# Performance work log

Measured on AMD Instinct MI355X. Metric: run time of the kernel, lower is better.

The kernel has to match this reference:

```python
import jax, jax.numpy as jnp
import numpy as np

D = 128      # entity_and_theorem_embedding_size
M = 8192     # nodes per tree level
L = 5        # internal (non-leaf) levels
V = 4096     # number of input entities (leaf vocab)
K = 8        # number of binary numerical functions
KL = 4       # number of binary logic functions
G = 4096     # number of ground-truth logic statements


def setup_inputs() -> dict:
    key = jax.random.key(0)
    ks = jax.random.split(key, 16)
    s = 0.05
    return {
        "leaf_ids": jax.random.randint(ks[0], (M,), 0, V, dtype=jnp.int32),
        "left_idx": jax.random.randint(ks[1], (L, M), 0, M, dtype=jnp.int32),
        "right_idx": jax.random.randint(ks[2], (L, M), 0, M, dtype=jnp.int32),
        "nf_fid": jax.random.randint(ks[3], (L, M), 0, K, dtype=jnp.int32),
        "gt_left": jax.random.randint(ks[4], (G,), 0, M, dtype=jnp.int32),
        "gt_right": jax.random.randint(ks[5], (G,), 0, M, dtype=jnp.int32),
        "lf_fid": jax.random.randint(ks[6], (G,), 0, KL, dtype=jnp.int32),
        "emb": jax.random.normal(ks[7], (V, D), jnp.float32),
        "W1": jax.random.normal(ks[8], (K, 2 * D, 4 * D), jnp.float32) * s,
        "b1": jnp.zeros((K, 4 * D), jnp.float32),
        "W2": jax.random.normal(ks[9], (K, 4 * D, 2 * D), jnp.float32) * s,
        "b2": jnp.zeros((K, 2 * D), jnp.float32),
        "W3": jax.random.normal(ks[10], (K, 2 * D, D), jnp.float32) * s,
        "b3": jnp.zeros((K, D), jnp.float32),
        "Wl1": jax.random.normal(ks[11], (KL, 2 * D, 4 * D), jnp.float32) * s,
        "bl1": jnp.zeros((KL, 4 * D), jnp.float32),
        "Wl2": jax.random.normal(ks[12], (KL, 4 * D, D), jnp.float32) * s,
        "bl2": jnp.zeros((KL, D), jnp.float32),
    }


def _select(y, fid):
    # y: [N, K, F], fid: [N] -> [N, F]  (per-node dynamic MLP dispatch)
    return jnp.take_along_axis(y, fid[:, None, None], axis=1)[:, 0, :]


def reference(leaf_ids, left_idx, right_idx, nf_fid, gt_left, gt_right, lf_fid,
              emb, W1, b1, W2, b2, W3, b3, Wl1, bl1, Wl2, bl2):
    # Leaf entities: embedding lookup (input_entity_embedding)
    h0 = emb[leaf_ids]  # [M, D]

    # Internal entity nodes: recursive nf_two2one MLPs, level-synchronous
    def level(h, xs):
        li, ri, fid = xs
        x = jnp.concatenate([h[li], h[ri]], axis=-1)          # [M, 2D] concat of operands
        a1 = jax.nn.relu(jnp.einsum('nd,kdf->nkf', x, W1) + b1)   # [M, K, 4D]
        a2 = jax.nn.relu(jnp.einsum('nkd,kdf->nkf', a1, W2) + b2) # [M, K, 2D]
        a3 = jnp.einsum('nkd,kdf->nkf', a2, W3) + b3              # [M, K, D]
        return _select(a3, fid), None
    hL, _ = jax.lax.scan(level, h0, (left_idx, right_idx, nf_fid))

    # Logic statements: lf_two2one MLP on pairs of entity encodings
    xg = jnp.concatenate([hL[gt_left], hL[gt_right]], axis=-1)    # [G, 2D]
    g1 = jax.nn.relu(jnp.einsum('nd,kdf->nkf', xg, Wl1) + bl1)    # [G, KL, 4D]
    g2 = jnp.einsum('nkd,kdf->nkf', g1, Wl2) + bl2                # [G, KL, D]
    return _select(g2, lf_fid)                                    # [G, D]
```

## Files before the change

### kernel.cpp

```cpp
#include <hip/hip_runtime.h>

constexpr int D  = 128;
constexpr int M  = 8192;
constexpr int L  = 5;
constexpr int K  = 8;
constexpr int KL = 4;
constexpr int G  = 4096;

constexpr int TB   = 64;
constexpr int PADL = M + K * TB;
constexpr int PADG = G + KL * TB;

typedef short bf16x8 __attribute__((ext_vector_type(8)));
typedef float f32x4  __attribute__((ext_vector_type(4)));

__device__ __forceinline__ unsigned short f2bf(float x) {
  union { float f; unsigned int u; } c; c.f = x;
  unsigned int u = c.u + 0x7FFF + ((c.u >> 16) & 1);
  return (unsigned short)(u >> 16);
}
__device__ __forceinline__ float bf2f(unsigned short h) {
  union { unsigned int u; float f; } c; c.u = ((unsigned int)h) << 16;
  return c.f;
}

__global__ void leaf_gather_kernel(const int* __restrict__ leaf_ids,
                                   const float* __restrict__ emb,
                                   short* __restrict__ hs) {
  int idx = blockIdx.x * 256 + threadIdx.x;
  int n = idx >> 7, d = idx & 127;
  float w = emb[(size_t)leaf_ids[n] * D + d];
  unsigned short hh = f2bf(w);
  hs[n * 256 + d]       = (short)hh;
  hs[n * 256 + 128 + d] = (short)f2bf(w - bf2f(hh));
}

__global__ void bucket64_kernel(const int* __restrict__ nf_fid,
                                const int* __restrict__ lf_fid,
                                int* __restrict__ orders) {
  int b = blockIdx.x;
  const int* fid; int N, Kf, cap; int* out;
  if (b < L) { fid = nf_fid + b * M; N = M; Kf = K;  cap = PADL; out = orders + b * PADL; }
  else       { fid = lf_fid;         N = G; Kf = KL; cap = PADG; out = orders + L * PADL; }
  __shared__ int cnt[8];
  __shared__ int cur[8];
  int tid = threadIdx.x;
  if (tid < Kf) cnt[tid] = 0;
  __syncthreads();
  for (int i = tid; i < N; i += 256) atomicAdd(&cnt[fid[i]], 1);
  __syncthreads();
  if (tid == 0) {
    int off = 0;
    for (int k = 0; k < Kf; ++k) { cur[k] = off; off += ((cnt[k] + TB - 1) / TB) * TB; }
  }
  __syncthreads();
  for (int i = tid; i < cap; i += 256) out[i] = -1;
  __syncthreads();
  for (int i = tid; i < N; i += 256) {
    int kk = fid[i];
    int pos = atomicAdd(&cur[kk], 1);
    out[pos] = i;
  }
}

__global__ void prep_kernel(const float* __restrict__ W1, const float* __restrict__ W2,
                            const float* __restrict__ W3, const float* __restrict__ Wl1,
                            const float* __restrict__ Wl2,
                            short* __restrict__ B1T, short* __restrict__ B2T,
                            short* __restrict__ B3T, short* __restrict__ BL1T,
                            short* __restrict__ BL2T) {
  int b = blockIdx.x;
  const float* W; short* BT; int KD, F;
  if      (b < 4096) { W = W1;  BT = B1T;  KD = 256; F = 512; }
  else if (b < 6144) { W = W2;  BT = B2T;  KD = 512; F = 256; b -= 4096; }
  else if (b < 7168) { W = W3;  BT = B3T;  KD = 256; F = 128; b -= 6144; }
  else if (b < 9216) { W = Wl1; BT = BL1T; KD = 256; F = 512; b -= 7168; }
  else               { W = Wl2; BT = BL2T; KD = 512; F = 128; b -= 9216; }
  int k = b / F, f = b % F;
  for (int d = threadIdx.x; d < KD; d += 256) {
    float w = W[((size_t)k * KD + d) * F + f];
    unsigned short hi = f2bf(w);
    unsigned short lo = f2bf(w - bf2f(hi));
    BT[((size_t)k * F + f) * (2 * KD) + d]      = (short)hi;
    BT[((size_t)k * F + f) * (2 * KD) + KD + d] = (short)lo;
  }
}

template<int KH, int NN, int EPI, int FUSED>
__global__ __launch_bounds__(256, 3) void mfma_gemm(
    const short* __restrict__ A, const short* __restrict__ hsrc,
    const int* __restrict__ gl, const int* __restrict__ gr,
    const short* __restrict__ BT, const float* __restrict__ bias,
    short* __restrict__ Aout, float* __restrict__ outp,
    const int* __restrict__ order, const int* __restrict__ fid) {
  constexpr int BK    = 64;
  constexpr int NCH   = 3 * KH / BK;
  constexpr int LDA   = BK + 8;
  constexpr int TROWS = 32;
  __shared__ __align__(16) short As[2][TROWS * LDA];
  __shared__ __align__(16) short Bs[2][128 * LDA];
  __shared__ int nodesS[TROWS], liS[TROWS], riS[TROWS];

  const int tid  = threadIdx.x;
  const int row0 = blockIdx.x * TROWS;
  const int ct   = blockIdx.y;

  if (tid < TROWS) {
    int node = order[row0 + tid];
    nodesS[tid] = node;
    if (FUSED) {
      liS[tid] = node >= 0 ? gl[node] : 0;
      riS[tid] = node >= 0 ? gr[node] : 0;
    }
  }
  __syncthreads();
  if (nodesS[0] < 0) return;
  const int kfn = fid[nodesS[0]];
  const short* __restrict__ Bk = BT + (size_t)kfn * NN * (2 * KH);

  const int lane = tid & 63, wave = tid >> 6;
  const int wr = (wave >> 1) * 16;
  const int wc = wave & 1;
  const int l15 = lane & 15, oct = lane >> 4;

  const int ar = tid >> 3;
  const int ag = (tid & 7) * 8;
  const int bn = tid >> 1;
  const int bg = (tid & 1) * 32;

  f32x4 acc[4];
  #pragma unroll
  for (int j = 0; j < 4; ++j) acc[j] = (f32x4)0.f;

  auto loadB_to = [&](int c, int4& r0, int4& r1, int4& r2, int4& r3) {
    int ko = c * BK, seg = ko / KH, wi = ko % KH;
    int pb = (seg == 2) ? KH + wi : wi;
    const int4* p = (const int4*)(Bk + (size_t)(ct * 128 + bn) * (2 * KH) + pb + bg);
    r0 = p[0]; r1 = p[1]; r2 = p[2]; r3 = p[3];
  };
  auto loadA_to = [&](int c, int4& r0) {
    int ko = c * BK, seg = ko / KH, wi = ko % KH;
    int pa = ((seg == 1) ? KH : 0) + wi + ag;
    if (FUSED) {
      int s4 = pa >> 7;
      int node = (s4 & 1) ? riS[ar] : liS[ar];
      if (nodesS[ar] >= 0) {
        r0 = *(const int4*)(hsrc + (size_t)node * 256 + ((s4 >> 1) << 7) + (pa & 127));
      } else {
        r0 = make_int4(0, 0, 0, 0);
      }
    } else {
      r0 = *(const int4*)(A + (size_t)(row0 + ar) * (2 * KH) + pa);
    }
  };
  auto storeA = [&](int b, const int4& r0) {
    *(int4*)&As[b][ar * LDA + ag] = r0;
  };
  auto storeB = [&](int b, const int4& r0, const int4& r1, const int4& r2, const int4& r3) {
    int4* db = (int4*)&Bs[b][bn * LDA + bg];
    db[0] = r0; db[1] = r1; db[2] = r2; db[3] = r3;
  };
  auto compute = [&](int b) {
    __builtin_amdgcn_s_setprio(1);
    #pragma unroll
    for (int s = 0; s < 2; ++s) {
      const int ko = s * 32 + oct * 8;
      bf16x8 afr = *(const bf16x8*)&As[b][(wr + l15) * LDA + ko];
      #pragma unroll
      for (int cf = 0; cf < 4; ++cf) {
        bf16x8 bb = *(const bf16x8*)&Bs[b][(wc * 64 + cf * 16 + l15) * LDA + ko];
        acc[cf] = __builtin_amdgcn_mfma_f32_16x16x32_bf16(afr, bb, acc[cf], 0, 0, 0);
      }
    }
    __builtin_amdgcn_s_setprio(0);
  };

  int4 a0, a1, b00, b01, b02, b03, b10, b11, b12, b13;
  loadA_to(0, a0); loadB_to(0, b00, b01, b02, b03);
  loadA_to(1, a1); loadB_to(1, b10, b11, b12, b13);
  storeA(0, a0); storeB(0, b00, b01, b02, b03);
  __syncthreads();
  for (int c = 0; c < NCH; c += 2) {
    storeA(1, a1); storeB(1, b10, b11, b12, b13);
    if (c + 2 < NCH) { loadA_to(c + 2, a0); loadB_to(c + 2, b00, b01, b02, b03); }
    compute(0);
    __syncthreads();
    if (c + 2 < NCH) { storeA(0, a0); storeB(0, b00, b01, b02, b03); }
    if (c + 3 < NCH) { loadA_to(c + 3, a1); loadB_to(c + 3, b10, b11, b12, b13); }
    compute(1);
    __syncthreads();
  }

  if (EPI == 0) {
    short* Ls = (short*)&Bs[0][0];
    #pragma unroll
    for (int part = 0; part < 2; ++part) {
      __syncthreads();
      #pragma unroll
      for (int cf = 0; cf < 4; ++cf) {
        int colL = wc * 64 + cf * 16 + l15;
        float bv = bias[kfn * NN + ct * 128 + colL];
        #pragma unroll
        for (int j = 0; j < 4; ++j) {
          int row = wr + oct * 4 + j;
          float v = fmaxf(acc[cf][j] + bv, 0.f);
          unsigned short hh = f2bf(v);
          unsigned short val = (part == 0) ? hh : f2bf(v - bf2f(hh));
          Ls[row * 128 + colL] = (short)val;
        }
      }
      __syncthreads();
      int row = tid >> 3, sg = (tid & 7) * 16;
      const int4* src = (const int4*)&Ls[row * 128 + sg];
      int4* dst = (int4*)&Aout[(size_t)(row0 + row) * (2 * NN) + part * NN + ct * 128 + sg];
      dst[0] = src[0]; dst[1] = src[1];
    }
  } else if (EPI == 1) {
    float* Lf = (float*)&Bs[0][0];
    #pragma unroll
    for (int h = 0; h < 2; ++h) {
      __syncthreads();
      if (wc == h) {
        #pragma unroll
        for (int cf = 0; cf < 4; ++cf) {
          int colL = cf * 16 + l15;
          float bv = bias[kfn * 128 + h * 64 + colL];
          #pragma unroll
          for (int j = 0; j < 4; ++j) {
            int row = wr + oct * 4 + j;
            Lf[row * 64 + colL] = acc[cf][j] + bv;
          }
        }
      }
      __syncthreads();
      int row = tid >> 3, off = (tid & 7) * 8;
      int node = nodesS[row];
      if (node >= 0) {
        const float4* src = (const float4*)&Lf[row * 64 + off];
        float4* dst = (float4*)&outp[(size_t)node * 128 + h * 64 + off];
        dst[0] = src[0]; dst[1] = src[1];
      }
    }
  } else {
    short* Ls = (short*)&Bs[0][0];
    #pragma unroll
    for (int cf = 0; cf < 4; ++cf) {
      int colL = wc * 64 + cf * 16 + l15;
      float bv = bias[kfn * 128 + colL];
      #pragma unroll
      for (int j = 0; j < 4; ++j) {
        int row = wr + oct * 4 + j;
        float v = acc[cf][j] + bv;
        unsigned short hh = f2bf(v);
        Ls[row * 256 + colL]       = (short)hh;
        Ls[row * 256 + 128 + colL] = (short)f2bf(v - bf2f(hh));
      }
    }
    __syncthreads();
    int row = tid >> 3, sg = (tid & 7) * 32;
    int node = nodesS[row];
    if (node >= 0) {
      const int4* src = (const int4*)&Ls[row * 256 + sg];
      int4* dst = (int4*)&Aout[(size_t)node * 256 + sg];
      dst[0] = src[0]; dst[1] = src[1]; dst[2] = src[2]; dst[3] = src[3];
    }
  }
}

extern "C" void kernel_launch(void* const* d_in, const int* in_sizes, int n_in,
                              void* d_out, int out_size, void* d_ws, size_t ws_size,
                              hipStream_t stream) {
  const int*   leaf_ids  = (const int*)d_in[0];
  const int*   left_idx  = (const int*)d_in[1];
  const int*   right_idx = (const int*)d_in[2];
  const int*   nf_fid    = (const int*)d_in[3];
  const int*   gt_left   = (const int*)d_in[4];
  const int*   gt_right  = (const int*)d_in[5];
  const int*   lf_fid    = (const int*)d_in[6];
  const float* emb       = (const float*)d_in[7];
  const float* W1 = (const float*)d_in[8];
  const float* b1 = (const float*)d_in[9];
  const float* W2 = (const float*)d_in[10];
  const float* b2 = (const float*)d_in[11];
  const float* W3 = (const float*)d_in[12];
  const float* b3 = (const float*)d_in[13];
  const float* Wl1 = (const float*)d_in[14];
  const float* bl1 = (const float*)d_in[15];
  const float* Wl2 = (const float*)d_in[16];
  const float* bl2 = (const float*)d_in[17];
  float* out = (float*)d_out;

  const size_t SZ_H    = (size_t)M * 256 * 2;
  const size_t SZ_A1   = (size_t)PADL * 1024 * 2;
  const size_t SZ_A2   = (size_t)PADL * 512 * 2;
  const size_t SZ_B1T  = (size_t)8 * 512 * 512 * 2;
  const size_t SZ_B2T  = (size_t)8 * 256 * 1024 * 2;
  const size_t SZ_B3T  = (size_t)8 * 128 * 512 * 2;
  const size_t SZ_BL1T = (size_t)4 * 512 * 512 * 2;
  const size_t SZ_BL2T = (size_t)4 * 128 * 1024 * 2;

  char* p = (char*)d_ws;
  short* hsA  = (short*)p;  p += SZ_H;
  short* hsB  = (short*)p;  p += SZ_H;
  short* a1s  = (short*)p;  p += SZ_A1;
  short* a2s  = (short*)p;  p += SZ_A2;
  short* B1T  = (short*)p;  p += SZ_B1T;
  short* B2T  = (short*)p;  p += SZ_B2T;
  short* B3T  = (short*)p;  p += SZ_B3T;
  short* BL1T = (short*)p;  p += SZ_BL1T;
  short* BL2T = (short*)p;  p += SZ_BL2T;
  int*   orders = (int*)p;

  leaf_gather_kernel<<<(M * D) / 256, 256, 0, stream>>>(leaf_ids, emb, hsA);
  bucket64_kernel<<<L + 1, 256, 0, stream>>>(nf_fid, lf_fid, orders);
  prep_kernel<<<9728, 256, 0, stream>>>(W1, W2, W3, Wl1, Wl2,
                                        B1T, B2T, B3T, BL1T, BL2T);

  short* hin = hsA;
  short* hout = hsB;
  for (int l = 0; l < L; ++l) {
    const int* ord = orders + l * PADL;
    const int* fidl = nf_fid + l * M;
    mfma_gemm<256, 512, 0, 1><<<dim3(PADL / 32, 4), 256, 0, stream>>>(
        nullptr, hin, left_idx + l * M, right_idx + l * M,
        B1T, b1, a1s, nullptr, ord, fidl);
    mfma_gemm<512, 256, 0, 0><<<dim3(PADL / 32, 2), 256, 0, stream>>>(
        a1s, nullptr, nullptr, nullptr,
        B2T, b2, a2s, nullptr, ord, fidl);
    mfma_gemm<256, 128, 2, 0><<<dim3(PADL / 32, 1), 256, 0, stream>>>(
        a2s, nullptr, nullptr, nullptr,
        B3T, b3, hout, nullptr, ord, fidl);
    short* t = hin; hin = hout; hout = t;
  }
  const int* ordG = orders + L * PADL;
  mfma_gemm<256, 512, 0, 1><<<dim3(PADG / 32, 4), 256, 0, stream>>>(
      nullptr, hin, gt_left, gt_right,
      BL1T, bl1, a1s, nullptr, ordG, lf_fid);
  mfma_gemm<512, 128, 1, 0><<<dim3(PADG / 32, 1), 256, 0, stream>>>(
      a1s, nullptr, nullptr, nullptr,
      BL2T, bl2, nullptr, out, ordG, lf_fid);
}
```

Baseline: 462.7 us.

## Use 64-row tiles for large GEMMs and swizzle blocks across XCDs

Makes the row-tile height a template parameter and uses 64-row tiles, with two MFMA row fragments per wave, for the first two GEMMs of each level and for the first logic GEMM. Each loaded B tile is reused across twice as many rows, which halves weight traffic per output. The occupancy hint for these kernels drops from 3 to 2 blocks. Block indices are also remapped so that consecutive row tiles, which usually share a function's weights, land on the same XCD to improve L2 reuse. The risks are fewer blocks in flight, higher register pressure, and the 64-row tile relying on the existing 64-row bucket padding.

```diff
diff --git a/kernel.cpp b/kernel.cpp
--- a/kernel.cpp
+++ b/kernel.cpp
@@ -22,6 +22,11 @@
 __device__ __forceinline__ float bf2f(unsigned short h) {
   union { unsigned int u; float f; } c; c.u = ((unsigned int)h) << 16;
   return c.f;
+}
+
+__device__ __forceinline__ int xcd_swizzle(int b, int n) {
+  int q = n >> 3, r = n & 7, xcd = b & 7, off = b >> 3;
+  return (xcd < r ? xcd * (q + 1) : r * (q + 1) + (xcd - r) * q) + off;
 }
 
 __global__ void leaf_gather_kernel(const int* __restrict__ leaf_ids,
@@ -86,8 +91,8 @@
   }
 }
 
-template<int KH, int NN, int EPI, int FUSED>
-__global__ __launch_bounds__(256, 3) void mfma_gemm(
+template<int KH, int NN, int EPI, int FUSED, int TROWS>
+__global__ __launch_bounds__(256, TROWS == 64 ? 2 : 3) void mfma_gemm(
     const short* __restrict__ A, const short* __restrict__ hsrc,
     const int* __restrict__ gl, const int* __restrict__ gr,
     const short* __restrict__ BT, const float* __restrict__ bias,
@@ -96,13 +101,15 @@
   constexpr int BK    = 64;
   constexpr int NCH   = 3 * KH / BK;
   constexpr int LDA   = BK + 8;
-  constexpr int TROWS = 32;
+  constexpr int RF    = TROWS / 32;
+  constexpr int TPR   = 256 / TROWS;
   __shared__ __align__(16) short As[2][TROWS * LDA];
   __shared__ __align__(16) short Bs[2][128 * LDA];
   __shared__ int nodesS[TROWS], liS[TROWS], riS[TROWS];
 
   const int tid  = threadIdx.x;
-  const int row0 = blockIdx.x * TROWS;
+  const int bx   = xcd_swizzle(blockIdx.x, gridDim.x);
+  const int row0 = bx * TROWS;
   const int ct   = blockIdx.y;
 
   if (tid < TROWS) {
@@ -119,18 +126,20 @@
   const short* __restrict__ Bk = BT + (size_t)kfn * NN * (2 * KH);
 
   const int lane = tid & 63, wave = tid >> 6;
-  const int wr = (wave >> 1) * 16;
+  const int wr = (wave >> 1) * (TROWS / 2);
   const int wc = wave & 1;
   const int l15 = lane & 15, oct = lane >> 4;
 
-  const int ar = tid >> 3;
-  const int ag = (tid & 7) * 8;
+  const int ar = tid / TPR;
+  const int ag = (tid % TPR) * (BK / TPR);
   const int bn = tid >> 1;
   const int bg = (tid & 1) * 32;
 
-  f32x4 acc[4];
+  f32x4 acc[RF][4];
   #pragma unroll
-  for (int j = 0; j < 4; ++j) acc[j] = (f32x4)0.f;
+  for (int i = 0; i < RF; ++i)
+    #pragma unroll
+    for (int j = 0; j < 4; ++j) acc[i][j] = (f32x4)0.f;
 
   auto loadB_to = [&](int c, int4& r0, int4& r1, int4& r2, int4& r3) {
     int ko = c * BK, seg = ko / KH, wi = ko % KH;
@@ -138,23 +147,30 @@
     const int4* p = (const int4*)(Bk + (size_t)(ct * 128 + bn) * (2 * KH) + pb + bg);
     r0 = p[0]; r1 = p[1]; r2 = p[2]; r3 = p[3];
   };
-  auto loadA_to = [&](int c, int4& r0) {
+  auto loadA_to = [&](int c, int4& r0, int4& r1) {
     int ko = c * BK, seg = ko / KH, wi = ko % KH;
     int pa = ((seg == 1) ? KH : 0) + wi + ag;
     if (FUSED) {
       int s4 = pa >> 7;
       int node = (s4 & 1) ? riS[ar] : liS[ar];
       if (nodesS[ar] >= 0) {
-        r0 = *(const int4*)(hsrc + (size_t)node * 256 + ((s4 >> 1) << 7) + (pa & 127));
+        const int4* p = (const int4*)(hsrc + (size_t)node * 256 + ((s4 >> 1) << 7) + (pa & 127));
+        r0 = p[0];
+        if (TPR == 4) r1 = p[1];
       } else {
         r0 = make_int4(0, 0, 0, 0);
+        if (TPR == 4) r1 = make_int4(0, 0, 0, 0);
       }
     } else {
-      r0 = *(const int4*)(A + (size_t)(row0 + ar) * (2 * KH) + pa);
-    }
-  };
-  auto storeA = [&](int b, const int4& r0) {
-    *(int4*)&As[b][ar * LDA + ag] = r0;
+      const int4* p = (const int4*)(A + (size_t)(row0 + ar) * (2 * KH) + pa);
+      r0 = p[0];
+      if (TPR == 4) r1 = p[1];
+    }
+  };
+  auto storeA = [&](int b, const int4& r0, const int4& r1) {
+    int4* d4 = (int4*)&As[b][ar * LDA + ag];
+    d4[0] = r0;
+    if (TPR == 4) d4[1] = r1;
   };
   auto storeB = [&](int b, const int4& r0, const int4& r1, const int4& r2, const int4& r3) {
     int4* db = (int4*)&Bs[b][bn * LDA + bg];
@@ -165,28 +181,34 @@
     #pragma unroll
     for (int s = 0; s < 2; ++s) {
       const int ko = s * 32 + oct * 8;
-      bf16x8 afr = *(const bf16x8*)&As[b][(wr + l15) * LDA + ko];
+      bf16x8 afr[RF];
+      #pragma unroll
+      for (int rf = 0; rf < RF; ++rf)
+        afr[rf] = *(const bf16x8*)&As[b][(wr + rf * 16 + l15) * LDA + ko];
       #pragma unroll
       for (int cf = 0; cf < 4; ++cf) {
         bf16x8 bb = *(const bf16x8*)&Bs[b][(wc * 64 + cf * 16 + l15) * LDA + ko];
-        acc[cf] = __builtin_amdgcn_mfma_f32_16x16x32_bf16(afr, bb, acc[cf], 0, 0, 0);
+        #pragma unroll
+        for (int rf = 0; rf < RF; ++rf)
+          acc[rf][cf] = __builtin_amdgcn_mfma_f32_16x16x32_bf16(afr[rf], bb, acc[rf][cf], 0, 0, 0);
       }
     }
     __builtin_amdgcn_s_setprio(0);
   };
 
-  int4 a0, a1, b00, b01, b02, b03, b10, b11, b12, b13;
-  loadA_to(0, a0); loadB_to(0, b00, b01, b02, b03);
-  loadA_to(1, a1); loadB_to(1, b10, b11, b12, b13);
-  storeA(0, a0); storeB(0, b00, b01, b02, b03);
+  int4 a00, a01, a10, a11;
+  int4 b00, b01, b02, b03, b10, b11, b12, b13;
+  loadA_to(0, a00, a01); loadB_to(0, b00, b01, b02, b03);
+  loadA_to(1, a10, a11); loadB_to(1, b10, b11, b12, b13);
+  storeA(0, a00, a01); storeB(0, b00, b01, b02, b03);
   __syncthreads();
   for (int c = 0; c < NCH; c += 2) {
-    storeA(1, a1); storeB(1, b10, b11, b12, b13);
-    if (c + 2 < NCH) { loadA_to(c + 2, a0); loadB_to(c + 2, b00, b01, b02, b03); }
+    storeA(1, a10, a11); storeB(1, b10, b11, b12, b13);
+    if (c + 2 < NCH) { loadA_to(c + 2, a00, a01); loadB_to(c + 2, b00, b01, b02, b03); }
     compute(0);
     __syncthreads();
-    if (c + 2 < NCH) { storeA(0, a0); storeB(0, b00, b01, b02, b03); }
-    if (c + 3 < NCH) { loadA_to(c + 3, a1); loadB_to(c + 3, b10, b11, b12, b13); }
+    if (c + 2 < NCH) { storeA(0, a00, a01); storeB(0, b00, b01, b02, b03); }
+    if (c + 3 < NCH) { loadA_to(c + 3, a10, a11); loadB_to(c + 3, b10, b11, b12, b13); }
     compute(1);
     __syncthreads();
   }
@@ -197,23 +219,28 @@
     for (int part = 0; part < 2; ++part) {
       __syncthreads();
       #pragma unroll
-      for (int cf = 0; cf < 4; ++cf) {
-        int colL = wc * 64 + cf * 16 + l15;
-        float bv = bias[kfn * NN + ct * 128 + colL];
-        #pragma unroll
-        for (int j = 0; j < 4; ++j) {
-          int row = wr + oct * 4 + j;
-          float v = fmaxf(acc[cf][j] + bv, 0.f);
-          unsigned short hh = f2bf(v);
-          unsigned short val = (part == 0) ? hh : f2bf(v - bf2f(hh));
-          Ls[row * 128 + colL] = (short)val;
+      for (int rf = 0; rf < RF; ++rf)
+        #pragma unroll
+        for (int cf = 0; cf < 4; ++cf) {
+          int colL = wc * 64 + cf * 16 + l15;
+          float bv = bias[kfn * NN + ct * 128 + colL];
+          #pragma unroll
+          for (int j = 0; j < 4; ++j) {
+            int row = wr + rf * 16 + oct * 4 + j;
+            float v = fmaxf(acc[rf][cf][j] + bv, 0.f);
+            unsigned short hh = f2bf(v);
+            unsigned short val = (part == 0) ? hh : f2bf(v - bf2f(hh));
+            Ls[row * 128 + colL] = (short)val;
+          }
         }
-      }
       __syncthreads();
-      int row = tid >> 3, sg = (tid & 7) * 16;
+      constexpr int SPT = TROWS / 2;
+      constexpr int TPW = 128 / SPT;
+      int row = tid / TPW, sg = (tid % TPW) * SPT;
       const int4* src = (const int4*)&Ls[row * 128 + sg];
       int4* dst = (int4*)&Aout[(size_t)(row0 + row) * (2 * NN) + part * NN + ct * 128 + sg];
-      dst[0] = src[0]; dst[1] = src[1];
+      #pragma unroll
+      for (int q = 0; q < SPT / 8; ++q) dst[q] = src[q];
     }
   } else if (EPI == 1) {
     float* Lf = (float*)&Bs[0][0];
@@ -222,47 +249,57 @@
       __syncthreads();
       if (wc == h) {
         #pragma unroll
-        for (int cf = 0; cf < 4; ++cf) {
-          int colL = cf * 16 + l15;
-          float bv = bias[kfn * 128 + h * 64 + colL];
+        for (int rf = 0; rf < RF; ++rf)
           #pragma unroll
-          for (int j = 0; j < 4; ++j) {
-            int row = wr + oct * 4 + j;
-            Lf[row * 64 + colL] = acc[cf][j] + bv;
+          for (int cf = 0; cf < 4; ++cf) {
+            int colL = cf * 16 + l15;
+            float bv = bias[kfn * 128 + h * 64 + colL];
+            #pragma unroll
+            for (int j = 0; j < 4; ++j) {
+              int row = wr + rf * 16 + oct * 4 + j;
+              Lf[row * 64 + colL] = acc[rf][cf][j] + bv;
+            }
           }
-        }
       }
       __syncthreads();
-      int row = tid >> 3, off = (tid & 7) * 8;
+      constexpr int FPT = TROWS / 4;
+      constexpr int TPW = 64 / FPT;
+      int row = tid / TPW, off = (tid % TPW) * FPT;
       int node = nodesS[row];
       if (node >= 0) {
         const float4* src = (const float4*)&Lf[row * 64 + off];
         float4* dst = (float4*)&outp[(size_t)node * 128 + h * 64 + off];
-        dst[0] = src[0]; dst[1] = src[1];
+        #pragma unroll
+        for (int q = 0; q < FPT / 4; ++q) dst[q] = src[q];
       }
     }
   } else {
     short* Ls = (short*)&Bs[0][0];
     #pragma unroll
-    for (int cf = 0; cf < 4; ++cf) {
-      int colL = wc * 64 + cf * 16 + l15;
-      float bv = bias[kfn * 128 + colL];
-      #pragma unroll
-      for (int j = 0; j < 4; ++j) {
-        int row = wr + oct * 4 + j;
-        float v = acc[cf][j] + bv;
-        unsigned short hh = f2bf(v);
-        Ls[row * 256 + colL]       = (short)hh;
-        Ls[row * 256 + 128 + colL] = (short)f2bf(v - bf2f(hh));
-      }
-    }
+    for (int rf = 0; rf < RF; ++rf)
+      #pragma unroll
+      for (int cf = 0; cf < 4; ++cf) {
+        int colL = wc * 64 + cf * 16 + l15;
+        float bv = bias[kfn * 128 + colL];
+        #pragma unroll
+        for (int j = 0; j < 4; ++j) {
+          int row = wr + rf * 16 + oct * 4 + j;
+          float v = acc[rf][cf][j] + bv;
+          unsigned short hh = f2bf(v);
+          Ls[row * 256 + colL]       = (short)hh;
+          Ls[row * 256 + 128 + colL] = (short)f2bf(v - bf2f(hh));
+        }
+      }
     __syncthreads();
-    int row = tid >> 3, sg = (tid & 7) * 32;
+    constexpr int SPT = 256 * TROWS / 256;
+    constexpr int TPW = 256 / SPT;
+    int row = tid / TPW, sg = (tid % TPW) * SPT;
     int node = nodesS[row];
     if (node >= 0) {
       const int4* src = (const int4*)&Ls[row * 256 + sg];
       int4* dst = (int4*)&Aout[(size_t)node * 256 + sg];
-      dst[0] = src[0]; dst[1] = src[1]; dst[2] = src[2]; dst[3] = src[3];
+      #pragma unroll
+      for (int q = 0; q < SPT / 8; ++q) dst[q] = src[q];
     }
   }
 }
@@ -321,22 +358,22 @@
   for (int l = 0; l < L; ++l) {
     const int* ord = orders + l * PADL;
     const int* fidl = nf_fid + l * M;
-    mfma_gemm<256, 512, 0, 1><<<dim3(PADL / 32, 4), 256, 0, stream>>>(
+    mfma_gemm<256, 512, 0, 1, 64><<<dim3(PADL / 64, 4), 256, 0, stream>>>(
         nullptr, hin, left_idx + l * M, right_idx + l * M,
         B1T, b1, a1s, nullptr, ord, fidl);
-    mfma_gemm<512, 256, 0, 0><<<dim3(PADL / 32, 2), 256, 0, stream>>>(
+    mfma_gemm<512, 256, 0, 0, 64><<<dim3(PADL / 64, 2), 256, 0, stream>>>(
         a1s, nullptr, nullptr, nullptr,
         B2T, b2, a2s, nullptr, ord, fidl);
-    mfma_gemm<256, 128, 2, 0><<<dim3(PADL / 32, 1), 256, 0, stream>>>(
+    mfma_gemm<256, 128, 2, 0, 32><<<dim3(PADL / 32, 1), 256, 0, stream>>>(
         a2s, nullptr, nullptr, nullptr,
         B3T, b3, hout, nullptr, ord, fidl);
     short* t = hin; hin = hout; hout = t;
   }
   const int* ordG = orders + L * PADL;
-  mfma_gemm<256, 512, 0, 1><<<dim3(PADG / 32, 4), 256, 0, stream>>>(
+  mfma_gemm<256, 512, 0, 1, 64><<<dim3(PADG / 64, 4), 256, 0, stream>>>(
       nullptr, hin, gt_left, gt_right,
       BL1T, bl1, a1s, nullptr, ordG, lf_fid);
-  mfma_gemm<512, 128, 1, 0><<<dim3(PADG / 32, 1), 256, 0, stream>>>(
+  mfma_gemm<512, 128, 1, 0, 32><<<dim3(PADG / 32, 1), 256, 0, stream>>>(
       a1s, nullptr, nullptr, nullptr,
       BL2T, bl2, nullptr, out, ordG, lf_fid);
 }
```

New measurement: 462.3 us. No clear change (-0.1%).

## Fuse three-layer per-level MLP into one kernel keeping activations in LDS

Applied to the files above, without the earlier changes.

Replaces the three separate GEMM launches per tree level (and two for the logic MLP) with one fused kernel per level. Each 32-row tile gathers its operand pairs into shared memory and runs all layers there, so the intermediate activations never go to global memory. It also adds an XCD-aware block swizzle. In exchange each block is much larger (about 100KB of LDS, launch bounds of 1) and the grid shrinks to one column tile per row tile, which lowers occupancy and parallelism.

```diff
diff --git a/kernel.cpp b/kernel.cpp
--- a/kernel.cpp
+++ b/kernel.cpp
@@ -22,6 +22,11 @@
 __device__ __forceinline__ float bf2f(unsigned short h) {
   union { unsigned int u; float f; } c; c.u = ((unsigned int)h) << 16;
   return c.f;
+}
+
+__device__ __forceinline__ int xcd_swizzle(int b, int n) {
+  int q = n >> 3, r = n & 7, xcd = b & 7, off = b >> 3;
+  return (xcd < r ? xcd * (q + 1) : r * (q + 1) + (xcd - r) * q) + off;
 }
 
 __global__ void leaf_gather_kernel(const int* __restrict__ leaf_ids,
@@ -86,137 +91,156 @@
   }
 }
 
-template<int KH, int NN, int EPI, int FUSED>
-__global__ __launch_bounds__(256, 3) void mfma_gemm(
-    const short* __restrict__ A, const short* __restrict__ hsrc,
+template<bool LOGIC>
+__global__ __launch_bounds__(256, 1) void fused_level(
+    const short* __restrict__ hsrc,
     const int* __restrict__ gl, const int* __restrict__ gr,
-    const short* __restrict__ BT, const float* __restrict__ bias,
-    short* __restrict__ Aout, float* __restrict__ outp,
+    const short* __restrict__ B1, const float* __restrict__ bias1,
+    const short* __restrict__ B2, const float* __restrict__ bias2,
+    const short* __restrict__ B3, const float* __restrict__ bias3,
+    short* __restrict__ hs_out, float* __restrict__ outp,
     const int* __restrict__ order, const int* __restrict__ fid) {
-  constexpr int BK    = 64;
-  constexpr int NCH   = 3 * KH / BK;
-  constexpr int LDA   = BK + 8;
   constexpr int TROWS = 32;
-  __shared__ __align__(16) short As[2][TROWS * LDA];
-  __shared__ __align__(16) short Bs[2][128 * LDA];
+  constexpr int LDB  = 72;
+  constexpr int LDX  = 520;
+  constexpr int LDA1 = 1032;
+  __shared__ __align__(16) short Xs[TROWS * LDX];
+  __shared__ __align__(16) short A1s[TROWS * LDA1];
+  __shared__ __align__(16) short Bsh[2][128 * LDB];
   __shared__ int nodesS[TROWS], liS[TROWS], riS[TROWS];
 
   const int tid  = threadIdx.x;
-  const int row0 = blockIdx.x * TROWS;
-  const int ct   = blockIdx.y;
+  const int bx   = xcd_swizzle(blockIdx.x, gridDim.x);
+  const int row0 = bx * TROWS;
 
   if (tid < TROWS) {
     int node = order[row0 + tid];
     nodesS[tid] = node;
-    if (FUSED) {
-      liS[tid] = node >= 0 ? gl[node] : 0;
-      riS[tid] = node >= 0 ? gr[node] : 0;
-    }
+    liS[tid] = node >= 0 ? gl[node] : 0;
+    riS[tid] = node >= 0 ? gr[node] : 0;
   }
   __syncthreads();
   if (nodesS[0] < 0) return;
   const int kfn = fid[nodesS[0]];
-  const short* __restrict__ Bk = BT + (size_t)kfn * NN * (2 * KH);
+
+  {
+    int r = tid >> 3, q = tid & 7;
+    const short* sl = hsrc + (size_t)liS[r] * 256;
+    const short* sr = hsrc + (size_t)riS[r] * 256;
+    int4* dst = (int4*)&Xs[r * LDX];
+    #pragma unroll
+    for (int q4 = 0; q4 < 4; ++q4) {
+      const int4* s = (const int4*)(((q4 & 1) ? sr : sl) + (q4 >> 1) * 128 + q * 16);
+      dst[q4 * 16 + q * 2 + 0] = s[0];
+      dst[q4 * 16 + q * 2 + 1] = s[1];
+    }
+  }
 
   const int lane = tid & 63, wave = tid >> 6;
   const int wr = (wave >> 1) * 16;
   const int wc = wave & 1;
   const int l15 = lane & 15, oct = lane >> 4;
-
-  const int ar = tid >> 3;
-  const int ag = (tid & 7) * 8;
   const int bn = tid >> 1;
   const int bg = (tid & 1) * 32;
 
   f32x4 acc[4];
-  #pragma unroll
-  for (int j = 0; j < 4; ++j) acc[j] = (f32x4)0.f;
-
-  auto loadB_to = [&](int c, int4& r0, int4& r1, int4& r2, int4& r3) {
-    int ko = c * BK, seg = ko / KH, wi = ko % KH;
-    int pb = (seg == 2) ? KH + wi : wi;
-    const int4* p = (const int4*)(Bk + (size_t)(ct * 128 + bn) * (2 * KH) + pb + bg);
-    r0 = p[0]; r1 = p[1]; r2 = p[2]; r3 = p[3];
+
+  auto run_phase = [&](const short* Asrc_, int ldaA, int KHp, int NNp,
+                       const short* Bk, const float* biask,
+                       short* Dst_, int ldaD) {
+    const int NCH  = 3 * KHp / 64;
+    const int ncts = NNp >> 7;
+    for (int ct = 0; ct < ncts; ++ct) {
+      #pragma unroll
+      for (int j = 0; j < 4; ++j) acc[j] = (f32x4)0.f;
+      int4 t0[4], t1[4];
+      auto loadB = [&](int4* t, int c) {
+        int ko = c * 64;
+        int pb = (ko < KHp) ? ko : ko - KHp;
+        const int4* p = (const int4*)(Bk + (size_t)(ct * 128 + bn) * (2 * KHp) + pb + bg);
+        t[0] = p[0]; t[1] = p[1]; t[2] = p[2]; t[3] = p[3];
+      };
+      auto storeB = [&](int b, int4* t) {
+        int4* db = (int4*)&Bsh[b][bn * LDB + bg];
+        db[0] = t[0]; db[1] = t[1]; db[2] = t[2]; db[3] = t[3];
+      };
+      auto computeC = [&](int b, int c) {
+        int ko0 = c * 64;
+        int paA = (ko0 < 2 * KHp) ? ko0 : ko0 - 2 * KHp;
+        __builtin_amdgcn_s_setprio(1);
+        #pragma unroll
+        for (int s = 0; s < 2; ++s) {
+          int ko = s * 32 + oct * 8;
+          bf16x8 afr = *(const bf16x8*)&Asrc_[(wr + l15) * ldaA + paA + ko];
+          #pragma unroll
+          for (int cf = 0; cf < 4; ++cf) {
+            bf16x8 bb = *(const bf16x8*)&Bsh[b][(wc * 64 + cf * 16 + l15) * LDB + ko];
+            acc[cf] = __builtin_amdgcn_mfma_f32_16x16x32_bf16(afr, bb, acc[cf], 0, 0, 0);
+          }
+        }
+        __builtin_amdgcn_s_setprio(0);
+      };
+      loadB(t0, 0); loadB(t1, 1);
+      __syncthreads();
+      storeB(0, t0);
+      __syncthreads();
+      for (int c = 0; c < NCH; c += 2) {
+        storeB(1, t1);
+        if (c + 2 < NCH) loadB(t0, c + 2);
+        computeC(0, c);
+        __syncthreads();
+        if (c + 2 < NCH) storeB(0, t0);
+        if (c + 3 < NCH) loadB(t1, c + 3);
+        computeC(1, c + 1);
+        __syncthreads();
+      }
+      if (Dst_) {
+        #pragma unroll
+        for (int cf = 0; cf < 4; ++cf) {
+          int colL = wc * 64 + cf * 16 + l15;
+          float bv = biask[kfn * NNp + ct * 128 + colL];
+          #pragma unroll
+          for (int j = 0; j < 4; ++j) {
+            int row = wr + oct * 4 + j;
+            float v = fmaxf(acc[cf][j] + bv, 0.f);
+            unsigned short hh = f2bf(v);
+            Dst_[row * ldaD + ct * 128 + colL]       = (short)hh;
+            Dst_[row * ldaD + NNp + ct * 128 + colL] = (short)f2bf(v - bf2f(hh));
+          }
+        }
+      }
+    }
   };
-  auto loadA_to = [&](int c, int4& r0) {
-    int ko = c * BK, seg = ko / KH, wi = ko % KH;
-    int pa = ((seg == 1) ? KH : 0) + wi + ag;
-    if (FUSED) {
-      int s4 = pa >> 7;
-      int node = (s4 & 1) ? riS[ar] : liS[ar];
-      if (nodesS[ar] >= 0) {
-        r0 = *(const int4*)(hsrc + (size_t)node * 256 + ((s4 >> 1) << 7) + (pa & 127));
-      } else {
-        r0 = make_int4(0, 0, 0, 0);
-      }
-    } else {
-      r0 = *(const int4*)(A + (size_t)(row0 + ar) * (2 * KH) + pa);
-    }
-  };
-  auto storeA = [&](int b, const int4& r0) {
-    *(int4*)&As[b][ar * LDA + ag] = r0;
-  };
-  auto storeB = [&](int b, const int4& r0, const int4& r1, const int4& r2, const int4& r3) {
-    int4* db = (int4*)&Bs[b][bn * LDA + bg];
-    db[0] = r0; db[1] = r1; db[2] = r2; db[3] = r3;
-  };
-  auto compute = [&](int b) {
-    __builtin_amdgcn_s_setprio(1);
+
+  run_phase(Xs, LDX, 256, 512, B1 + (size_t)kfn * 512 * 512, bias1, A1s, LDA1);
+  if (!LOGIC) {
+    run_phase(A1s, LDA1, 512, 256, B2 + (size_t)kfn * 256 * 1024, bias2, Xs, LDX);
+    run_phase(Xs, LDX, 256, 128, B3 + (size_t)kfn * 128 * 512, bias3, nullptr, 0);
+    short* Ls = (short*)&Bsh[0][0];
     #pragma unroll
-    for (int s = 0; s < 2; ++s) {
-      const int ko = s * 32 + oct * 8;
-      bf16x8 afr = *(const bf16x8*)&As[b][(wr + l15) * LDA + ko];
+    for (int cf = 0; cf < 4; ++cf) {
+      int colL = wc * 64 + cf * 16 + l15;
+      float bv = bias3[kfn * 128 + colL];
       #pragma unroll
-      for (int cf = 0; cf < 4; ++cf) {
-        bf16x8 bb = *(const bf16x8*)&Bs[b][(wc * 64 + cf * 16 + l15) * LDA + ko];
-        acc[cf] = __builtin_amdgcn_mfma_f32_16x16x32_bf16(afr, bb, acc[cf], 0, 0, 0);
-      }
-    }
-    __builtin_amdgcn_s_setprio(0);
-  };
-
-  int4 a0, a1, b00, b01, b02, b03, b10, b11, b12, b13;
-  loadA_to(0, a0); loadB_to(0, b00, b01, b02, b03);
-  loadA_to(1, a1); loadB_to(1, b10, b11, b12, b13);
-  storeA(0, a0); storeB(0, b00, b01, b02, b03);
-  __syncthreads();
-  for (int c = 0; c < NCH; c += 2) {
-    storeA(1, a1); storeB(1, b10, b11, b12, b13);
-    if (c + 2 < NCH) { loadA_to(c + 2, a0); loadB_to(c + 2, b00, b01, b02, b03); }
-    compute(0);
+      for (int j = 0; j < 4; ++j) {
+        int row = wr + oct * 4 + j;
+        float v = acc[cf][j] + bv;
+        unsigned short hh = f2bf(v);
+        Ls[row * 256 + colL]       = (short)hh;
+        Ls[row * 256 + 128 + colL] = (short)f2bf(v - bf2f(hh));
+      }
+    }
     __syncthreads();
-    if (c + 2 < NCH) { storeA(0, a0); storeB(0, b00, b01, b02, b03); }
-    if (c + 3 < NCH) { loadA_to(c + 3, a1); loadB_to(c + 3, b10, b11, b12, b13); }
-    compute(1);
-    __syncthreads();
-  }
-
-  if (EPI == 0) {
-    short* Ls = (short*)&Bs[0][0];
-    #pragma unroll
-    for (int part = 0; part < 2; ++part) {
-      __syncthreads();
-      #pragma unroll
-      for (int cf = 0; cf < 4; ++cf) {
-        int colL = wc * 64 + cf * 16 + l15;
-        float bv = bias[kfn * NN + ct * 128 + colL];
-        #pragma unroll
-        for (int j = 0; j < 4; ++j) {
-          int row = wr + oct * 4 + j;
-          float v = fmaxf(acc[cf][j] + bv, 0.f);
-          unsigned short hh = f2bf(v);
-          unsigned short val = (part == 0) ? hh : f2bf(v - bf2f(hh));
-          Ls[row * 128 + colL] = (short)val;
-        }
-      }
-      __syncthreads();
-      int row = tid >> 3, sg = (tid & 7) * 16;
-      const int4* src = (const int4*)&Ls[row * 128 + sg];
-      int4* dst = (int4*)&Aout[(size_t)(row0 + row) * (2 * NN) + part * NN + ct * 128 + sg];
-      dst[0] = src[0]; dst[1] = src[1];
-    }
-  } else if (EPI == 1) {
-    float* Lf = (float*)&Bs[0][0];
+    int row = tid >> 3, sg = (tid & 7) * 32;
+    int node = nodesS[row];
+    if (node >= 0) {
+      const int4* src = (const int4*)&Ls[row * 256 + sg];
+      int4* dst = (int4*)&hs_out[(size_t)node * 256 + sg];
+      dst[0] = src[0]; dst[1] = src[1]; dst[2] = src[2]; dst[3] = src[3];
+    }
+  } else {
+    run_phase(A1s, LDA1, 512, 128, B2 + (size_t)kfn * 128 * 1024, bias2, nullptr, 0);
+    float* Lf = (float*)&Bsh[0][0];
     #pragma unroll
     for (int h = 0; h < 2; ++h) {
       __syncthreads();
@@ -224,7 +248,7 @@
         #pragma unroll
         for (int cf = 0; cf < 4; ++cf) {
           int colL = cf * 16 + l15;
-          float bv = bias[kfn * 128 + h * 64 + colL];
+          float bv = bias2[kfn * 128 + h * 64 + colL];
           #pragma unroll
           for (int j = 0; j < 4; ++j) {
             int row = wr + oct * 4 + j;
@@ -240,29 +264,6 @@
         float4* dst = (float4*)&outp[(size_t)node * 128 + h * 64 + off];
         dst[0] = src[0]; dst[1] = src[1];
       }
-    }
-  } else {
-    short* Ls = (short*)&Bs[0][0];
-    #pragma unroll
-    for (int cf = 0; cf < 4; ++cf) {
-      int colL = wc * 64 + cf * 16 + l15;
-      float bv = bias[kfn * 128 + colL];
-      #pragma unroll
-      for (int j = 0; j < 4; ++j) {
-        int row = wr + oct * 4 + j;
-        float v = acc[cf][j] + bv;
-        unsigned short hh = f2bf(v);
-        Ls[row * 256 + colL]       = (short)hh;
-        Ls[row * 256 + 128 + colL] = (short)f2bf(v - bf2f(hh));
-      }
-    }
-    __syncthreads();
-    int row = tid >> 3, sg = (tid & 7) * 32;
-    int node = nodesS[row];
-    if (node >= 0) {
-      const int4* src = (const int4*)&Ls[row * 256 + sg];
-      int4* dst = (int4*)&Aout[(size_t)node * 256 + sg];
-      dst[0] = src[0]; dst[1] = src[1]; dst[2] = src[2]; dst[3] = src[3];
     }
   }
 }
@@ -291,8 +292,6 @@
   float* out = (float*)d_out;
 
   const size_t SZ_H    = (size_t)M * 256 * 2;
-  const size_t SZ_A1   = (size_t)PADL * 1024 * 2;
-  const size_t SZ_A2   = (size_t)PADL * 512 * 2;
   const size_t SZ_B1T  = (size_t)8 * 512 * 512 * 2;
   const size_t SZ_B2T  = (size_t)8 * 256 * 1024 * 2;
   const size_t SZ_B3T  = (size_t)8 * 128 * 512 * 2;
@@ -302,8 +301,6 @@
   char* p = (char*)d_ws;
   short* hsA  = (short*)p;  p += SZ_H;
   short* hsB  = (short*)p;  p += SZ_H;
-  short* a1s  = (short*)p;  p += SZ_A1;
-  short* a2s  = (short*)p;  p += SZ_A2;
   short* B1T  = (short*)p;  p += SZ_B1T;
   short* B2T  = (short*)p;  p += SZ_B2T;
   short* B3T  = (short*)p;  p += SZ_B3T;
@@ -319,24 +316,14 @@
   short* hin = hsA;
   short* hout = hsB;
   for (int l = 0; l < L; ++l) {
-    const int* ord = orders + l * PADL;
-    const int* fidl = nf_fid + l * M;
-    mfma_gemm<256, 512, 0, 1><<<dim3(PADL / 32, 4), 256, 0, stream>>>(
-        nullptr, hin, left_idx + l * M, right_idx + l * M,
-        B1T, b1, a1s, nullptr, ord, fidl);
-    mfma_gemm<512, 256, 0, 0><<<dim3(PADL / 32, 2), 256, 0, stream>>>(
-        a1s, nullptr, nullptr, nullptr,
-        B2T, b2, a2s, nullptr, ord, fidl);
-    mfma_gemm<256, 128, 2, 0><<<dim3(PADL / 32, 1), 256, 0, stream>>>(
-        a2s, nullptr, nullptr, nullptr,
-        B3T, b3, hout, nullptr, ord, fidl);
+    fused_level<false><<<PADL / 32, 256, 0, stream>>>(
+        hin, left_idx + l * M, right_idx + l * M,
+        B1T, b1, B2T, b2, B3T, b3,
+        hout, nullptr, orders + l * PADL, nf_fid + l * M);
     short* t = hin; hin = hout; hout = t;
   }
-  const int* ordG = orders + L * PADL;
-  mfma_gemm<256, 512, 0, 1><<<dim3(PADG / 32, 4), 256, 0, stream>>>(
-      nullptr, hin, gt_left, gt_right,
-      BL1T, bl1, a1s, nullptr, ordG, lf_fid);
-  mfma_gemm<512, 128, 1, 0><<<dim3(PADG / 32, 1), 256, 0, stream>>>(
-      a1s, nullptr, nullptr, nullptr,
-      BL2T, bl2, nullptr, out, ordG, lf_fid);
-}
+  fused_level<true><<<PADG / 32, 256, 0, stream>>>(
+      hin, gt_left, gt_right,
+      BL1T, bl1, BL2T, bl2, nullptr, nullptr,
+      nullptr, out, orders + L * PADL, lf_fid);
+}
```

After: 1.401 ms. +202.8%, slower.
